# Performance work log

Measured on AMD Instinct MI355X. Metric: run time of the kernel, lower is better.

The kernel has to match this reference:

```python
import jax, jax.numpy as jnp
import numpy as np

N_NODES = 50000
N_EDGES = 800000
HEADS = 4
OUT_CH = 64
NEG_SLOPE = 0.2  # PyG GATConv default


def gat_conv(x, edge_index, W, att_src, att_dst, bias):
    """PyG GATConv (concat=True, add_self_loops=True, eval mode).
    x: [N, F_in], edge_index: [2, E] (row 0 = src, row 1 = dst).
    W: [F_in, H*C], att_src/att_dst: [1, H, C], bias: [H*C].
    """
    n = x.shape[0]
    loops = jnp.arange(n, dtype=edge_index.dtype)
    src = jnp.concatenate([edge_index[0], loops])  # [E+N]
    dst = jnp.concatenate([edge_index[1], loops])

    h = (x @ W).reshape(n, HEADS, OUT_CH)           # [N, H, C]
    a_src = jnp.sum(h * att_src, axis=-1)           # [N, H]
    a_dst = jnp.sum(h * att_dst, axis=-1)           # [N, H]

    e = a_src[src] + a_dst[dst]                     # [E+N, H]
    e = jax.nn.leaky_relu(e, NEG_SLOPE)

    # segment softmax over incoming edges of each dst node
    e_max = jax.ops.segment_max(e, dst, num_segments=n)   # [N, H]
    e_exp = jnp.exp(e - e_max[dst])
    denom = jax.ops.segment_sum(e_exp, dst, num_segments=n)
    alpha = e_exp / (denom[dst] + 1e-16)            # [E+N, H]

    msg = h[src] * alpha[:, :, None]                # [E+N, H, C]
    out = jax.ops.segment_sum(msg, dst, num_segments=n)   # [N, H, C]
    return out.reshape(n, HEADS * OUT_CH) + bias


def setup_inputs() -> dict:
    key = jax.random.key(0)
    ks = jax.random.split(key, 10)
    d_in = 256
    d_hid = HEADS * OUT_CH  # 256
    s_in = 1.0 / np.sqrt(d_in)
    s_hid = 1.0 / np.sqrt(d_hid)
    return {
        "x": jax.random.normal(ks[0], (N_NODES, d_in), dtype=jnp.float32),
        "edge_index": jax.random.randint(ks[1], (2, N_EDGES), 0, N_NODES, dtype=jnp.int32),
        "W1": jax.random.normal(ks[2], (d_in, d_hid), dtype=jnp.float32) * s_in,
        "att_src1": jax.random.normal(ks[3], (1, HEADS, OUT_CH), dtype=jnp.float32) * s_hid,
        "att_dst1": jax.random.normal(ks[4], (1, HEADS, OUT_CH), dtype=jnp.float32) * s_hid,
        "b1": jnp.zeros((d_hid,), dtype=jnp.float32),
        "W2": jax.random.normal(ks[5], (d_hid, d_hid), dtype=jnp.float32) * s_hid,
        "att_src2": jax.random.normal(ks[6], (1, HEADS, OUT_CH), dtype=jnp.float32) * s_hid,
        "att_dst2": jax.random.normal(ks[7], (1, HEADS, OUT_CH), dtype=jnp.float32) * s_hid,
        "b2": jnp.zeros((d_hid,), dtype=jnp.float32),
    }


def reference(x, edge_index, W1, att_src1, att_dst1, b1, W2, att_src2, att_dst2, b2):
    # layer 1 + ELU (dropout is identity in eval mode)
    h = gat_conv(x, edge_index, W1, att_src1, att_dst1, b1)
    h = jax.nn.elu(h)
    # layer 2 + ELU
    h = gat_conv(h, edge_index, W2, att_src2, att_dst2, b2)
    h = jax.nn.elu(h)
    return h
```

## Files before the change

### kernel.cpp

```cpp
#include <hip/hip_runtime.h>
#include <hip/hip_bf16.h>

#define N_NODES 50000
#define N_EDGES 800000

typedef __attribute__((ext_vector_type(8))) short short8;
typedef __attribute__((ext_vector_type(4))) float floatx4;
typedef __attribute__((ext_vector_type(2))) uint uintx2;

__device__ __forceinline__ ushort f2bf(float f) {
    uint u = __float_as_uint(f);
    uint r = u + 0x7FFFu + ((u >> 16) & 1u);
    return (ushort)(r >> 16);
}
__device__ __forceinline__ float bfu2f(ushort h) {
    return __uint_as_float(((uint)h) << 16);
}
__device__ __forceinline__ float bflo(uint u) { return __uint_as_float(u << 16); }
__device__ __forceinline__ float bfhi(uint u) { return __uint_as_float(u & 0xffff0000u); }
__device__ __forceinline__ float lrelu(float e) { return e >= 0.f ? e : 0.2f * e; }

__global__ void deg_kernel(const int* __restrict__ dst, int* __restrict__ cnt, int E) {
    int i = blockIdx.x * blockDim.x + threadIdx.x;
    if (i < E) atomicAdd(&cnt[dst[i]], 1);
}

__global__ __launch_bounds__(256) void scan1_kernel(const int* __restrict__ cnt,
                                                    int* __restrict__ excl,
                                                    int* __restrict__ partial, int n) {
    __shared__ int sd[256];
    int tid = threadIdx.x;
    int i = blockIdx.x * 256 + tid;
    int v = (i < n) ? cnt[i] : 0;
    sd[tid] = v;
    __syncthreads();
    #pragma unroll
    for (int off = 1; off < 256; off <<= 1) {
        int t = (tid >= off) ? sd[tid - off] : 0;
        __syncthreads();
        sd[tid] += t;
        __syncthreads();
    }
    if (i < n) excl[i] = sd[tid] - v;
    if (tid == 255) partial[blockIdx.x] = sd[255];
}

__global__ __launch_bounds__(256) void scan2_kernel(int* __restrict__ partial, int nb) {
    __shared__ int sd[256];
    int tid = threadIdx.x;
    int v = (tid < nb) ? partial[tid] : 0;
    sd[tid] = v;
    __syncthreads();
    #pragma unroll
    for (int off = 1; off < 256; off <<= 1) {
        int t = (tid >= off) ? sd[tid - off] : 0;
        __syncthreads();
        sd[tid] += t;
        __syncthreads();
    }
    if (tid < nb) partial[tid] = sd[tid] - v;
}

__global__ __launch_bounds__(256) void scan3_kernel(const int* __restrict__ excl,
                                                    const int* __restrict__ partial,
                                                    int* __restrict__ row_ptr,
                                                    int* __restrict__ row_tmp, int n) {
    int i = blockIdx.x * 256 + threadIdx.x;
    if (i < n) {
        int v = excl[i] + partial[blockIdx.x];
        row_ptr[i] = v;
        row_tmp[i] = v;
    }
    if (i == 0) row_ptr[n] = N_EDGES;
}

__global__ void scatter_kernel(const int* __restrict__ src, const int* __restrict__ dst,
                               int* __restrict__ row_tmp, int* __restrict__ sorted_src,
                               int* __restrict__ sorted_dst, int E) {
    int i = blockIdx.x * blockDim.x + threadIdx.x;
    if (i < E) {
        int d = dst[i];
        int p = atomicAdd(&row_tmp[d], 1);
        sorted_src[p] = src[i];
        sorted_dst[p] = d;
    }
}

__global__ __launch_bounds__(320) void prep_w(const float* __restrict__ W1,
                                              const float* __restrict__ W2,
                                              const float* __restrict__ as1,
                                              const float* __restrict__ ad1,
                                              const float* __restrict__ as2,
                                              const float* __restrict__ ad2,
                                              ushort* __restrict__ Wt1_hi,
                                              ushort* __restrict__ Wt1_lo,
                                              ushort* __restrict__ Wt2_hi,
                                              ushort* __restrict__ Wt2_lo) {
    int t = threadIdx.x, k = blockIdx.x & 255;
    int l1 = (blockIdx.x < 256);
    const float* W = l1 ? W1 : W2;
    const float* as_ = l1 ? as1 : as2;
    const float* ad_ = l1 ? ad1 : ad2;
    ushort* Wh = l1 ? Wt1_hi : Wt2_hi;
    ushort* Wl = l1 ? Wt1_lo : Wt2_lo;
    if (t < 256) {
        float v = W[k * 256 + t];
        ushort hb = f2bf(v);
        Wh[t * 256 + k] = hb;
        Wl[t * 256 + k] = f2bf(v - bfu2f(hb));
    } else if (t < 264) {
        int j = t - 256;
        int h = j & 3;
        const float* vec = (j < 4) ? as_ : ad_;
        float acc = 0.f;
        for (int c = 0; c < 64; c++) acc += W[k * 256 + h * 64 + c] * vec[h * 64 + c];
        ushort hb = f2bf(acc);
        Wh[t * 256 + k] = hb;
        Wl[t * 256 + k] = f2bf(acc - bfu2f(hb));
    } else if (t < 272) {
        Wh[t * 256 + k] = 0;
        Wl[t * 256 + k] = 0;
    }
}

__global__ __launch_bounds__(256) void gemm_att_kernel(const float* __restrict__ A,
                                                       const ushort* __restrict__ Wt_hi,
                                                       const ushort* __restrict__ Wt_lo,
                                                       const float* __restrict__ att_s,
                                                       const float* __restrict__ att_d,
                                                       ushort* __restrict__ H,
                                                       float* __restrict__ a_src,
                                                       float* __restrict__ a_dst, int M) {
    const int ROWP = 40;
    __shared__ ushort hi_s[128 * ROWP];
    __shared__ ushort lo_s[128 * ROWP];
    const int tid = threadIdx.x;
    const int wave = tid >> 6, lane = tid & 63;
    const int quad = lane >> 4, l16 = lane & 15;
    const int brow = blockIdx.x * 64;
    const int coff = blockIdx.y * 128;
    const int mrow = brow + wave * 16 + l16;
    const int mload = (mrow < M) ? mrow : (M - 1);

    floatx4 acc[8];
    #pragma unroll
    for (int t = 0; t < 8; t++) acc[t] = (floatx4){0.f, 0.f, 0.f, 0.f};

    for (int k0 = 0; k0 < 256; k0 += 32) {
        __syncthreads();
        {
            int t = tid & 127;
            const ushort* g = ((tid < 128) ? Wt_hi : Wt_lo) + (size_t)(coff + t) * 256 + k0;
            ushort* d = ((tid < 128) ? hi_s : lo_s) + t * ROWP;
            #pragma unroll
            for (int i = 0; i < 4; i++)
                *reinterpret_cast<short8*>(d + i * 8) =
                    *reinterpret_cast<const short8*>(g + i * 8);
        }
        __syncthreads();
        const float* ap = A + (size_t)mload * 256 + k0 + quad * 8;
        float4 a0 = *reinterpret_cast<const float4*>(ap);
        float4 a1 = *reinterpret_cast<const float4*>(ap + 4);
        float av[8] = {a0.x, a0.y, a0.z, a0.w, a1.x, a1.y, a1.z, a1.w};
        short8 a_hi, a_lo;
        #pragma unroll
        for (int j = 0; j < 8; j++) {
            ushort hb = f2bf(av[j]);
            a_hi[j] = (short)hb;
            a_lo[j] = (short)f2bf(av[j] - bfu2f(hb));
        }
        #pragma unroll
        for (int t = 0; t < 8; t++) {
            int roff = (t * 16 + l16) * ROWP + quad * 8;
            short8 b_hi = *reinterpret_cast<const short8*>(&hi_s[roff]);
            short8 b_lo = *reinterpret_cast<const short8*>(&lo_s[roff]);
            acc[t] = __builtin_amdgcn_mfma_f32_16x16x32_bf16(a_hi, b_hi, acc[t], 0, 0, 0);
            acc[t] = __builtin_amdgcn_mfma_f32_16x16x32_bf16(a_hi, b_lo, acc[t], 0, 0, 0);
            acc[t] = __builtin_amdgcn_mfma_f32_16x16x32_bf16(a_lo, b_hi, acc[t], 0, 0, 0);
        }
    }
    const int hb = blockIdx.y * 2;
    float ps[2][4] = {}, pd[2][4] = {};
    #pragma unroll
    for (int t = 0; t < 8; t++) {
        int hh = t >> 2;
        float as_v = att_s[coff + t * 16 + l16];
        float ad_v = att_d[coff + t * 16 + l16];
        #pragma unroll
        for (int r = 0; r < 4; r++) {
            ps[hh][r] += acc[t][r] * as_v;
            pd[hh][r] += acc[t][r] * ad_v;
        }
    }
    #pragma unroll
    for (int off = 1; off < 16; off <<= 1) {
        #pragma unroll
        for (int hh = 0; hh < 2; hh++)
            #pragma unroll
            for (int r = 0; r < 4; r++) {
                ps[hh][r] += __shfl_xor(ps[hh][r], off, 64);
                pd[hh][r] += __shfl_xor(pd[hh][r], off, 64);
            }
    }
    if (l16 == 0) {
        #pragma unroll
        for (int r = 0; r < 4; r++) {
            int m = brow + wave * 16 + quad * 4 + r;
            if (m < M) {
                #pragma unroll
                for (int hh = 0; hh < 2; hh++) {
                    a_src[m * 4 + hb + hh] = ps[hh][r];
                    a_dst[m * 4 + hb + hh] = pd[hh][r];
                }
            }
        }
    }
    #pragma unroll
    for (int t = 0; t < 4; t++) {
        int c = t * 16 + l16;
        #pragma unroll
        for (int r = 0; r < 4; r++) {
            int m = brow + wave * 16 + quad * 4 + r;
            if (m < M) {
                uint pk = (uint)f2bf(acc[t][r]) | ((uint)f2bf(acc[t + 4][r]) << 16);
                *reinterpret_cast<uint*>(H + (size_t)m * 256 + c * 4 + hb) = pk;
            }
        }
    }
}

__global__ __launch_bounds__(256) void ew_kernel(const float* __restrict__ a_src,
                                                 const float* __restrict__ a_dst,
                                                 const int* __restrict__ sorted_src,
                                                 const int* __restrict__ sorted_dst,
                                                 float* __restrict__ ew, int E) {
    int j = blockIdx.x * 256 + threadIdx.x;
    if (j >= E) return;
    int s = sorted_src[j], d = sorted_dst[j];
    float4 as_ = *reinterpret_cast<const float4*>(a_src + (size_t)s * 4);
    float4 ad_ = *reinterpret_cast<const float4*>(a_dst + (size_t)d * 4);
    float4 w;
    w.x = __expf(lrelu(as_.x + ad_.x));
    w.y = __expf(lrelu(as_.y + ad_.y));
    w.z = __expf(lrelu(as_.z + ad_.z));
    w.w = __expf(lrelu(as_.w + ad_.w));
    *reinterpret_cast<float4*>(ew + (size_t)j * 4) = w;
}

#define AGG_ACC(W_, V_)                                                     \
    do {                                                                    \
        a0 += (W_).x * bflo((V_).x); a1 += (W_).y * bfhi((V_).x);           \
        a2 += (W_).z * bflo((V_).y); a3 += (W_).w * bfhi((V_).y);           \
        dp0 += (W_).x; dp1 += (W_).y; dp2 += (W_).z; dp3 += (W_).w;         \
    } while (0)

__global__ __launch_bounds__(256) void agg_kernel(const ushort* __restrict__ H,
                                                  const float* __restrict__ a_src,
                                                  const float* __restrict__ a_dst,
                                                  const int* __restrict__ row_ptr,
                                                  const int* __restrict__ sorted_src,
                                                  const float* __restrict__ ew,
                                                  const float* __restrict__ bias,
                                                  float* __restrict__ out, int N) {
    const int lane = threadIdx.x & 63;
    const int i = __builtin_amdgcn_readfirstlane(blockIdx.x * 4 + (threadIdx.x >> 6));
    if (i >= N) return;
    const float4 asv = *reinterpret_cast<const float4*>(a_src + (size_t)i * 4);
    const float4 adv = *reinterpret_cast<const float4*>(a_dst + (size_t)i * 4);
    const float ws0 = __expf(lrelu(asv.x + adv.x)), ws1 = __expf(lrelu(asv.y + adv.y));
    const float ws2 = __expf(lrelu(asv.z + adv.z)), ws3 = __expf(lrelu(asv.w + adv.w));
    const int start = row_ptr[i], end = row_ptr[i + 1];

    float a0 = 0.f, a1 = 0.f, a2 = 0.f, a3 = 0.f;
    float dp0 = 0.f, dp1 = 0.f, dp2 = 0.f, dp3 = 0.f;
    const ushort* __restrict__ Hl = H + lane * 4;

    for (int j0 = start; j0 < end; j0 += 8) {
        int s[8];
        #pragma unroll
        for (int k = 0; k < 8; k++) s[k] = sorted_src[j0 + k];
        floatx4 w[8];
        #pragma unroll
        for (int k = 0; k < 8; k++)
            w[k] = *reinterpret_cast<const floatx4*>(ew + (size_t)(j0 + k) * 4);
        uintx2 hv[8];
        #pragma unroll
        for (int k = 0; k < 8; k++)
            hv[k] = *reinterpret_cast<const uintx2*>(Hl + (size_t)s[k] * 256);
        if (j0 + 8 <= end) {
            #pragma unroll
            for (int k = 0; k < 8; k++) AGG_ACC(w[k], hv[k]);
        } else {
            #pragma unroll
            for (int k = 0; k < 8; k++)
                if (j0 + k < end) AGG_ACC(w[k], hv[k]);
        }
    }
    {
        uintx2 hv = *reinterpret_cast<const uintx2*>(Hl + (size_t)i * 256);
        a0 += ws0 * bflo(hv.x); a1 += ws1 * bfhi(hv.x);
        a2 += ws2 * bflo(hv.y); a3 += ws3 * bfhi(hv.y);
    }
    const float r0 = 1.f / (dp0 + ws0 + 1e-16f), r1 = 1.f / (dp1 + ws1 + 1e-16f);
    const float r2 = 1.f / (dp2 + ws2 + 1e-16f), r3 = 1.f / (dp3 + ws3 + 1e-16f);
    float* op = out + (size_t)i * 256 + lane;
    float v;
    v = a0 * r0 + bias[lane];        v = (v > 0.f) ? v : expm1f(v);
    __builtin_nontemporal_store(v, op);
    v = a1 * r1 + bias[64 + lane];   v = (v > 0.f) ? v : expm1f(v);
    __builtin_nontemporal_store(v, op + 64);
    v = a2 * r2 + bias[128 + lane];  v = (v > 0.f) ? v : expm1f(v);
    __builtin_nontemporal_store(v, op + 128);
    v = a3 * r3 + bias[192 + lane];  v = (v > 0.f) ? v : expm1f(v);
    __builtin_nontemporal_store(v, op + 192);
}

extern "C" void kernel_launch(void* const* d_in, const int* in_sizes, int n_in,
                              void* d_out, int out_size, void* d_ws, size_t ws_size,
                              hipStream_t stream) {
    const float* x      = (const float*)d_in[0];
    const int*   eidx   = (const int*)d_in[1];
    const float* W1     = (const float*)d_in[2];
    const float* att_s1 = (const float*)d_in[3];
    const float* att_d1 = (const float*)d_in[4];
    const float* b1     = (const float*)d_in[5];
    const float* W2     = (const float*)d_in[6];
    const float* att_s2 = (const float*)d_in[7];
    const float* att_d2 = (const float*)d_in[8];
    const float* b2     = (const float*)d_in[9];
    float* out = (float*)d_out;

    const int N = N_NODES, E = N_EDGES;
    char* ws = (char*)d_ws;
    size_t off = 0;
    auto alloc = [&](size_t bytes) -> void* {
        void* p = ws + off;
        off += (bytes + 255) & ~(size_t)255;
        return p;
    };
    ushort* h       = (ushort*)alloc((size_t)N * 256 * sizeof(ushort));
    float*  ew      = (float*) alloc((size_t)E * 4 * sizeof(float));
    float*  a_src   = (float*) alloc((size_t)N * 4 * sizeof(float));
    float*  a_dst   = (float*) alloc((size_t)N * 4 * sizeof(float));
    int*    cnt     = (int*)   alloc((size_t)N * sizeof(int));
    int*    row_ptr = (int*)   alloc((size_t)(N + 1) * sizeof(int));
    int*    row_tmp = (int*)   alloc((size_t)N * sizeof(int));
    int*    sorted  = (int*)   alloc((size_t)E * sizeof(int));
    int*    sortedd = (int*)   alloc((size_t)E * sizeof(int));
    int*    excl    = (int*)   alloc((size_t)N * sizeof(int));
    int*    partial = (int*)   alloc(256 * sizeof(int));
    ushort* Wt1_hi  = (ushort*)alloc(272 * 256 * sizeof(ushort));
    ushort* Wt1_lo  = (ushort*)alloc(272 * 256 * sizeof(ushort));
    ushort* Wt2_hi  = (ushort*)alloc(272 * 256 * sizeof(ushort));
    ushort* Wt2_lo  = (ushort*)alloc(272 * 256 * sizeof(ushort));
    float*  x2      = out;
    (void)ws_size; (void)in_sizes; (void)n_in; (void)out_size;

    const int* e_src = eidx;
    const int* e_dst = eidx + E;
    const int nsb = (N + 255) / 256;
    const int neb = (E + 255) / 256;

    prep_w<<<512, 320, 0, stream>>>(W1, W2, att_s1, att_d1, att_s2, att_d2,
                                    Wt1_hi, Wt1_lo, Wt2_hi, Wt2_lo);
    hipMemsetAsync(cnt, 0, N * sizeof(int), stream);
    deg_kernel<<<neb, 256, 0, stream>>>(e_dst, cnt, E);
    scan1_kernel<<<nsb, 256, 0, stream>>>(cnt, excl, partial, N);
    scan2_kernel<<<1, 256, 0, stream>>>(partial, nsb);
    scan3_kernel<<<nsb, 256, 0, stream>>>(excl, partial, row_ptr, row_tmp, N);
    scatter_kernel<<<neb, 256, 0, stream>>>(e_src, e_dst, row_tmp, sorted, sortedd, E);

    dim3 ggrid((N + 63) / 64, 2);
    int nblk = (N + 3) / 4;
    gemm_att_kernel<<<ggrid, 256, 0, stream>>>(x, Wt1_hi, Wt1_lo, att_s1, att_d1,
                                               h, a_src, a_dst, N);
    ew_kernel<<<neb, 256, 0, stream>>>(a_src, a_dst, sorted, sortedd, ew, E);
    agg_kernel<<<nblk, 256, 0, stream>>>(h, a_src, a_dst, row_ptr, sorted, ew, b1, x2, N);
    gemm_att_kernel<<<ggrid, 256, 0, stream>>>(x2, Wt2_hi, Wt2_lo, att_s2, att_d2,
                                               h, a_src, a_dst, N);
    ew_kernel<<<neb, 256, 0, stream>>>(a_src, a_dst, sorted, sortedd, ew, E);
    agg_kernel<<<nblk, 256, 0, stream>>>(h, a_src, a_dst, row_ptr, sorted, ew, b2, out, N);
}
```

Before: 458.7 us.

## Double-buffer weight tiles in LDS and prefetch A rows in GEMM

Reworks the GEMM+attention kernel's K loop to use two LDS buffers for the split-bf16 weight tiles. The next tile is loaded into registers during the current MFMA work, and A activations are prefetched two steps ahead. Each step now needs one barrier instead of two, and global load latency can overlap with compute. In exchange it doubles LDS use, which may reduce occupancy, and it uses more registers.

Result: no change. 450.2 us (-1.8%).

```diff
diff --git a/kernel.cpp b/kernel.cpp
--- a/kernel.cpp
+++ b/kernel.cpp
@@ -132,8 +132,8 @@
                                                        float* __restrict__ a_src,
                                                        float* __restrict__ a_dst, int M) {
     const int ROWP = 40;
-    __shared__ ushort hi_s[128 * ROWP];
-    __shared__ ushort lo_s[128 * ROWP];
+    __shared__ ushort hi_s[2][128 * ROWP];
+    __shared__ ushort lo_s[2][128 * ROWP];
     const int tid = threadIdx.x;
     const int wave = tid >> 6, lane = tid & 63;
     const int quad = lane >> 4, l16 = lane & 15;
@@ -146,22 +146,38 @@
     #pragma unroll
     for (int t = 0; t < 8; t++) acc[t] = (floatx4){0.f, 0.f, 0.f, 0.f};
 
-    for (int k0 = 0; k0 < 256; k0 += 32) {
-        __syncthreads();
-        {
-            int t = tid & 127;
-            const ushort* g = ((tid < 128) ? Wt_hi : Wt_lo) + (size_t)(coff + t) * 256 + k0;
-            ushort* d = ((tid < 128) ? hi_s : lo_s) + t * ROWP;
+    const int scol = tid & 127;
+    const ushort* gW = ((tid < 128) ? Wt_hi : Wt_lo) + (size_t)(coff + scol) * 256;
+    ushort* sB0 = ((tid < 128) ? &hi_s[0][0] : &lo_s[0][0]) + scol * ROWP;
+    ushort* sB1 = ((tid < 128) ? &hi_s[1][0] : &lo_s[1][0]) + scol * ROWP;
+
+    const float* ap = A + (size_t)mload * 256 + quad * 8;
+
+    short8 wreg[4];
+    #pragma unroll
+    for (int i = 0; i < 4; i++)
+        wreg[i] = *reinterpret_cast<const short8*>(gW + i * 8);
+    float4 af0[2], af1[2];
+    af0[0] = *reinterpret_cast<const float4*>(ap);
+    af1[0] = *reinterpret_cast<const float4*>(ap + 4);
+    af0[1] = *reinterpret_cast<const float4*>(ap + 32);
+    af1[1] = *reinterpret_cast<const float4*>(ap + 36);
+    #pragma unroll
+    for (int i = 0; i < 4; i++)
+        *reinterpret_cast<short8*>(sB0 + i * 8) = wreg[i];
+    asm volatile("s_waitcnt lgkmcnt(0)" ::: "memory");
+    __builtin_amdgcn_s_barrier();
+
+    #pragma unroll
+    for (int t = 0; t < 8; t++) {
+        const int cur = t & 1;
+        if (t < 7) {
             #pragma unroll
             for (int i = 0; i < 4; i++)
-                *reinterpret_cast<short8*>(d + i * 8) =
-                    *reinterpret_cast<const short8*>(g + i * 8);
-        }
-        __syncthreads();
-        const float* ap = A + (size_t)mload * 256 + k0 + quad * 8;
-        float4 a0 = *reinterpret_cast<const float4*>(ap);
-        float4 a1 = *reinterpret_cast<const float4*>(ap + 4);
-        float av[8] = {a0.x, a0.y, a0.z, a0.w, a1.x, a1.y, a1.z, a1.w};
+                wreg[i] = *reinterpret_cast<const short8*>(gW + (t + 1) * 32 + i * 8);
+        }
+        float av[8] = {af0[cur].x, af0[cur].y, af0[cur].z, af0[cur].w,
+                       af1[cur].x, af1[cur].y, af1[cur].z, af1[cur].w};
         short8 a_hi, a_lo;
         #pragma unroll
         for (int j = 0; j < 8; j++) {
@@ -169,15 +185,29 @@
             a_hi[j] = (short)hb;
             a_lo[j] = (short)f2bf(av[j] - bfu2f(hb));
         }
-        #pragma unroll
-        for (int t = 0; t < 8; t++) {
-            int roff = (t * 16 + l16) * ROWP + quad * 8;
-            short8 b_hi = *reinterpret_cast<const short8*>(&hi_s[roff]);
-            short8 b_lo = *reinterpret_cast<const short8*>(&lo_s[roff]);
-            acc[t] = __builtin_amdgcn_mfma_f32_16x16x32_bf16(a_hi, b_hi, acc[t], 0, 0, 0);
-            acc[t] = __builtin_amdgcn_mfma_f32_16x16x32_bf16(a_hi, b_lo, acc[t], 0, 0, 0);
-            acc[t] = __builtin_amdgcn_mfma_f32_16x16x32_bf16(a_lo, b_hi, acc[t], 0, 0, 0);
-        }
+        if (t < 6) {
+            af0[cur] = *reinterpret_cast<const float4*>(ap + (t + 2) * 32);
+            af1[cur] = *reinterpret_cast<const float4*>(ap + (t + 2) * 32 + 4);
+        }
+        const ushort* rh = (cur == 0) ? &hi_s[0][0] : &hi_s[1][0];
+        const ushort* rl = (cur == 0) ? &lo_s[0][0] : &lo_s[1][0];
+        #pragma unroll
+        for (int tt = 0; tt < 8; tt++) {
+            int roff = (tt * 16 + l16) * ROWP + quad * 8;
+            short8 b_hi = *reinterpret_cast<const short8*>(rh + roff);
+            short8 b_lo = *reinterpret_cast<const short8*>(rl + roff);
+            acc[tt] = __builtin_amdgcn_mfma_f32_16x16x32_bf16(a_hi, b_hi, acc[tt], 0, 0, 0);
+            acc[tt] = __builtin_amdgcn_mfma_f32_16x16x32_bf16(a_hi, b_lo, acc[tt], 0, 0, 0);
+            acc[tt] = __builtin_amdgcn_mfma_f32_16x16x32_bf16(a_lo, b_hi, acc[tt], 0, 0, 0);
+        }
+        if (t < 7) {
+            ushort* sBn = cur ? sB0 : sB1;
+            #pragma unroll
+            for (int i = 0; i < 4; i++)
+                *reinterpret_cast<short8*>(sBn + i * 8) = wreg[i];
+        }
+        asm volatile("s_waitcnt lgkmcnt(0)" ::: "memory");
+        __builtin_amdgcn_s_barrier();
     }
     const int hb = blockIdx.y * 2;
     float ps[2][4] = {}, pd[2][4] = {};
```
